# Kernel optimization log

Hardware: AMD Instinct MI355X
Metric: run time of the kernel (lower is better)

Reference implementation:

```python
import jax, jax.numpy as jnp
import numpy as np

B, P, D, H, U, C = 32, 196, 512, 8, 4, 500

def setup_inputs() -> dict:
    key = jax.random.key(0)
    ks = jax.random.split(key, 12)
    s = 0.02
    return {
        "patch_embeddings": jax.random.normal(ks[0], (B, P, D), jnp.float32),
        "global_features": jax.random.normal(ks[1], (B, D), jnp.float32),
        "query_vectors": jax.random.normal(ks[2], (H, D), jnp.float32) * s,
        "dom_W": jax.random.normal(ks[3], (D, D), jnp.float32) / np.sqrt(D),
        "dom_b": jnp.zeros((D,), jnp.float32),
        "sem_W": jax.random.normal(ks[4], (H, D, D), jnp.float32) / np.sqrt(D),
        "sem_b": jnp.zeros((H, D), jnp.float32),
        "unknown_semantic_tokens": jax.random.normal(ks[5], (U, D), jnp.float32) * s,
        "known_prefix": jax.random.normal(ks[6], (C, 1, D), jnp.float32) * s,   # SOS embedding per class
        "known_suffix": jax.random.normal(ks[7], (C, 1, D), jnp.float32) * s,   # last-token embedding per class
        "unk_prefix": jax.random.normal(ks[8], (1, D), jnp.float32) * s,
        "unk_suffix": jax.random.normal(ks[9], (1, D), jnp.float32) * s,
    }


def reference(patch_embeddings, global_features, query_vectors, dom_W, dom_b,
              sem_W, sem_b, unknown_semantic_tokens, known_prefix, known_suffix,
              unk_prefix, unk_suffix):
    b, p, d = patch_embeddings.shape
    h = query_vectors.shape[0]
    c = known_prefix.shape[0]
    u = unknown_semantic_tokens.shape[0]

    # SemanticTokenExtractor: per-head attention over patches (vectorized over heads)
    scores = jnp.einsum('bpd,hd->bph', patch_embeddings, query_vectors)      # [B,P,H]
    weights = jax.nn.softmax(scores, axis=1)                                  # softmax over patches
    semantic_tokens = jnp.einsum('bph,bpd->bhd', weights, patch_embeddings)   # [B,H,D]

    # DomainTokenGenerator (2D input -> identity) + domain projection (torch Linear: x @ W.T + b)
    projected_domain = global_features @ dom_W.T + dom_b                      # [B,D]

    # Per-head semantic projections: head k uses its own Linear
    projected_sem = jnp.einsum('bhd,hed->bhe', semantic_tokens, sem_W) + sem_b  # [B,H,D]

    # Known prompts: for each (b, c): [prefix_c(1), domain_b(1), semantics_b(H), suffix_c(1)]
    pre = jnp.broadcast_to(known_prefix[None], (b, c, 1, d))
    dom = jnp.broadcast_to(projected_domain[:, None, None, :], (b, c, 1, d))
    sem = jnp.broadcast_to(projected_sem[:, None], (b, c, h, d))
    suf = jnp.broadcast_to(known_suffix[None], (b, c, 1, d))
    known_prompts = jnp.concatenate([pre, dom, sem, suf], axis=2).reshape(b * c, h + 3, d)

    # Unknown prompts: [unk_prefix(1), domain_b(1), unknown_semantic_tokens(U), unk_suffix(1)]
    upre = jnp.broadcast_to(unk_prefix[None], (b, 1, d))
    udom = projected_domain[:, None, :]
    usem = jnp.broadcast_to(unknown_semantic_tokens[None], (b, u, d))
    usuf = jnp.broadcast_to(unk_suffix[None], (b, 1, d))
    unknown_prompts = jnp.concatenate([upre, udom, usem, usuf], axis=1)       # [B, U+3, D]

    return known_prompts, unknown_prompts, semantic_tokens
```

## Files before the change

kernel.cpp:

```cpp
#include <hip/hip_runtime.h>

typedef unsigned int uint32;
typedef uint32 v4u __attribute__((ext_vector_type(4)));

#define Bb 32
#define Pp 196
#define Dd 512
#define Hh 8
#define Uu 4
#define Cc 500

#define OUT1_ELEM_OFF 90112000
#define OUT2_ELEM_OFF 90226688

#define WS_SC   0
#define WS_PART 51200
#define WS_DOM  1099776
#define WS_SEM  1116160

__device__ __forceinline__ float dot4(float4 a, float4 b, float acc) {
    acc = fmaf(a.x, b.x, acc);
    acc = fmaf(a.y, b.y, acc);
    acc = fmaf(a.z, b.z, acc);
    acc = fmaf(a.w, b.w, acc);
    return acc;
}

__global__ __launch_bounds__(256)
void k_scores(const float* __restrict__ patch, const float* __restrict__ query,
              float* __restrict__ sc) {
    __shared__ float s_q[Hh * Dd];
    const int b = blockIdx.x / 49;
    const int p0 = (blockIdx.x % 49) * 4;
    const int tid = threadIdx.x;
    for (int j = tid; j < Hh * Dd / 4; j += 256)
        ((float4*)s_q)[j] = ((const float4*)query)[j];
    __syncthreads();

    const int wave = tid >> 6, lane = tid & 63;
    const int p = p0 + wave;
    const float* pr = patch + ((size_t)b * Pp + p) * Dd + lane * 8;
    const float4 v0 = *(const float4*)pr;
    const float4 v1 = *(const float4*)(pr + 4);

    float out = 0.f;
#pragma unroll
    for (int h = 0; h < 8; ++h) {
        const float4 q0 = *(const float4*)&s_q[h * Dd + lane * 8];
        const float4 q1 = *(const float4*)&s_q[h * Dd + lane * 8 + 4];
        float a = dot4(v0, q0, 0.f);
        a = dot4(v1, q1, a);
#pragma unroll
        for (int m = 32; m >= 1; m >>= 1) a += __shfl_xor(a, m, 64);
        if (lane == h) out = a;
    }
    if (lane < 8) sc[((size_t)b * Hh + lane) * Pp + p] = out;
}

__global__ __launch_bounds__(256)
void k_pool_part(const float* __restrict__ patch, const float* __restrict__ sc,
                 float* __restrict__ part) {
    __shared__ float s_w[Hh * Pp];
    const int b = blockIdx.x >> 3;
    const int pc = blockIdx.x & 7;
    const int tid = threadIdx.x;

    for (int j = tid; j < Hh * Pp; j += 256) s_w[j] = sc[(size_t)b * Hh * Pp + j];
    __syncthreads();

    {
        const int h = tid >> 5, gl = tid & 31;
        float m = -1e30f;
        for (int p = gl; p < Pp; p += 32) m = fmaxf(m, s_w[h * Pp + p]);
#pragma unroll
        for (int mm = 16; mm >= 1; mm >>= 1) m = fmaxf(m, __shfl_xor(m, mm, 64));
        float s = 0.f;
        for (int p = gl; p < Pp; p += 32) s += __expf(s_w[h * Pp + p] - m);
#pragma unroll
        for (int mm = 16; mm >= 1; mm >>= 1) s += __shfl_xor(s, mm, 64);
        const float inv = 1.f / s;
        for (int p = gl; p < Pp; p += 32)
            s_w[h * Pp + p] = __expf(s_w[h * Pp + p] - m) * inv;
    }
    __syncthreads();

    const int f = tid & 127;
    const int hq = tid >> 7;
    const int pstart = pc * 25;
    const int pend = (pstart + 25 < Pp) ? pstart + 25 : Pp;
    float4 a0 = {0, 0, 0, 0}, a1 = a0, a2 = a0, a3 = a0;
    const float4* pb4 = (const float4*)(patch + (size_t)b * Pp * Dd);
    for (int p = pstart; p < pend; ++p) {
        const float4 pv = pb4[p * 128 + f];
        const float w0 = s_w[(hq * 4 + 0) * Pp + p];
        const float w1 = s_w[(hq * 4 + 1) * Pp + p];
        const float w2 = s_w[(hq * 4 + 2) * Pp + p];
        const float w3 = s_w[(hq * 4 + 3) * Pp + p];
        a0.x = fmaf(w0, pv.x, a0.x); a0.y = fmaf(w0, pv.y, a0.y);
        a0.z = fmaf(w0, pv.z, a0.z); a0.w = fmaf(w0, pv.w, a0.w);
        a1.x = fmaf(w1, pv.x, a1.x); a1.y = fmaf(w1, pv.y, a1.y);
        a1.z = fmaf(w1, pv.z, a1.z); a1.w = fmaf(w1, pv.w, a1.w);
        a2.x = fmaf(w2, pv.x, a2.x); a2.y = fmaf(w2, pv.y, a2.y);
        a2.z = fmaf(w2, pv.z, a2.z); a2.w = fmaf(w2, pv.w, a2.w);
        a3.x = fmaf(w3, pv.x, a3.x); a3.y = fmaf(w3, pv.y, a3.y);
        a3.z = fmaf(w3, pv.z, a3.z); a3.w = fmaf(w3, pv.w, a3.w);
    }
    float4* po = (float4*)part + ((size_t)b * 8 + pc) * 1024;
    po[(hq * 4 + 0) * 128 + f] = a0;
    po[(hq * 4 + 1) * 128 + f] = a1;
    po[(hq * 4 + 2) * 128 + f] = a2;
    po[(hq * 4 + 3) * 128 + f] = a3;
}

__global__ __launch_bounds__(256)
void k_combine(const float* __restrict__ part, float* __restrict__ st) {
    const int idx = blockIdx.x * 256 + threadIdx.x;
    const int b = idx >> 10;
    const int r = idx & 1023;
    const float4* p4 = (const float4*)part;
    float4 a = {0, 0, 0, 0};
#pragma unroll
    for (int pc = 0; pc < 8; ++pc) {
        const float4 v = p4[((size_t)b * 8 + pc) * 1024 + r];
        a.x += v.x; a.y += v.y; a.z += v.z; a.w += v.w;
    }
    ((float4*)st)[idx] = a;
}

__global__ __launch_bounds__(256)
void k_proj(const float* __restrict__ gf, const float* __restrict__ domW,
            const float* __restrict__ domb, const float* __restrict__ semW,
            const float* __restrict__ semb, const float* __restrict__ st,
            float* __restrict__ dom_ws, float* __restrict__ sem_ws) {
    const int blk = blockIdx.x;
    if (blk < 512) {
        const int tg = blk * 256 + threadIdx.x;
        const int b = tg >> 12;
        const int rem = tg & 4095;
        const int h = rem >> 9;
        const int e = rem & 511;
        const float4* wr = (const float4*)(semW + (size_t)(h * Dd + e) * Dd);
        const float4* sr = (const float4*)(st + (size_t)(b * Hh + h) * Dd);
        float acc = semb[h * Dd + e];
#pragma unroll 8
        for (int j = 0; j < Dd / 4; ++j) acc = dot4(sr[j], wr[j], acc);
        sem_ws[(b * Hh + h) * Dd + e] = acc;
    } else {
        const int tg = (blk - 512) * 256 + threadIdx.x;
        const int b = tg >> 9;
        const int e = tg & 511;
        const float4* wr = (const float4*)(domW + (size_t)e * Dd);
        const float4* gr = (const float4*)(gf + (size_t)b * Dd);
        float acc = domb[e];
#pragma unroll 8
        for (int j = 0; j < Dd / 4; ++j) acc = dot4(gr[j], wr[j], acc);
        dom_ws[b * Dd + e] = acc;
    }
}

__global__ __launch_bounds__(256)
void k_assemble(const v4u* __restrict__ pre, const v4u* __restrict__ suf,
                const v4u* __restrict__ dom, const v4u* __restrict__ sem,
                const v4u* __restrict__ upre, const v4u* __restrict__ usuf,
                const v4u* __restrict__ ust,
                v4u* __restrict__ out0, v4u* __restrict__ out1) {
    const int blk = blockIdx.x;
    const int tid = threadIdx.x;
    if (blk < 1600) {
        const int b = blk / 50;
        const int chunk = blk % 50;
        __shared__ v4u mid[1152];
        for (int j = tid; j < 1152; j += 256)
            mid[j] = (j < 128) ? dom[b * 128 + j] : sem[b * 1024 + (j - 128)];
        __syncthreads();
        const int c0 = chunk * 10;
        for (int r = 0; r < 10; ++r) {
            const int c = c0 + r;
            v4u* row = out0 + (size_t)(b * Cc + c) * 1408;
            for (int i = tid; i < 1408; i += 256) {
                const int t = i >> 7;
                const int off = i & 127;
                v4u v;
                if (t == 0) v = pre[c * 128 + off];
                else if (t == 10) v = suf[c * 128 + off];
                else v = mid[(t - 1) * 128 + off];
                __builtin_nontemporal_store(v, &row[i]);
            }
        }
    } else {
        const int b = blk - 1600;
        for (int i = tid; i < 896; i += 256) {
            const int t = i >> 7;
            const int off = i & 127;
            v4u v;
            if (t == 0) v = upre[off];
            else if (t == 6) v = usuf[off];
            else if (t == 1) v = dom[b * 128 + off];
            else v = ust[(t - 2) * 128 + off];
            __builtin_nontemporal_store(v, &out1[b * 896 + i]);
        }
    }
}

extern "C" void kernel_launch(void* const* d_in, const int* in_sizes, int n_in,
                              void* d_out, int out_size, void* d_ws, size_t ws_size,
                              hipStream_t stream) {
    const float* patch = (const float*)d_in[0];
    const float* gf    = (const float*)d_in[1];
    const float* query = (const float*)d_in[2];
    const float* domW  = (const float*)d_in[3];
    const float* domb  = (const float*)d_in[4];
    const float* semW  = (const float*)d_in[5];
    const float* semb  = (const float*)d_in[6];
    const float* ust   = (const float*)d_in[7];
    const float* pre   = (const float*)d_in[8];
    const float* suf   = (const float*)d_in[9];
    const float* upre  = (const float*)d_in[10];
    const float* usuf  = (const float*)d_in[11];

    float* out = (float*)d_out;
    float* st_out = out + OUT2_ELEM_OFF;

    float* ws   = (float*)d_ws;
    float* sc_w = ws + WS_SC;
    float* part = ws + WS_PART;
    float* domp = ws + WS_DOM;
    float* semp = ws + WS_SEM;

    hipLaunchKernelGGL(k_scores, dim3(Bb * 49), dim3(256), 0, stream, patch, query, sc_w);
    hipLaunchKernelGGL(k_pool_part, dim3(Bb * 8), dim3(256), 0, stream, patch, sc_w, part);
    hipLaunchKernelGGL(k_combine, dim3(128), dim3(256), 0, stream, part, st_out);
    hipLaunchKernelGGL(k_proj, dim3(576), dim3(256), 0, stream,
                       gf, domW, domb, semW, semb, st_out, domp, semp);
    hipLaunchKernelGGL(k_assemble, dim3(1632), dim3(256), 0, stream,
                       (const v4u*)pre, (const v4u*)suf,
                       (const v4u*)domp, (const v4u*)semp,
                       (const v4u*)upre, (const v4u*)usuf, (const v4u*)ust,
                       (v4u*)out, (v4u*)(out + OUT1_ELEM_OFF));
}
```

Baseline: 480.4 us.

## Tile per-head projection through LDS and split pooling into more chunks

The per-head semantic projection now stages a 32-row slice of the head's weight matrix and all 32 batch semantic tokens in padded shared memory. Each thread computes a 2x2 register tile, so each weight is reused across all batches instead of being streamed once per batch from global memory. The pooling stage splits patches into 16 chunks per batch instead of 8, giving more blocks in exchange for more partial-sum traffic in the combine step. The large LDS footprint limits occupancy to one block per CU for the projection.

```diff
diff --git a/kernel.cpp b/kernel.cpp
--- a/kernel.cpp
+++ b/kernel.cpp
@@ -13,10 +13,12 @@
 #define OUT1_ELEM_OFF 90112000
 #define OUT2_ELEM_OFF 90226688
 
+#define NPC 16
+
 #define WS_SC   0
 #define WS_PART 51200
-#define WS_DOM  1099776
-#define WS_SEM  1116160
+#define WS_DOM  2148352
+#define WS_SEM  2164736
 
 __device__ __forceinline__ float dot4(float4 a, float4 b, float acc) {
     acc = fmaf(a.x, b.x, acc);
@@ -61,8 +63,8 @@
 void k_pool_part(const float* __restrict__ patch, const float* __restrict__ sc,
                  float* __restrict__ part) {
     __shared__ float s_w[Hh * Pp];
-    const int b = blockIdx.x >> 3;
-    const int pc = blockIdx.x & 7;
+    const int b = blockIdx.x >> 4;
+    const int pc = blockIdx.x & 15;
     const int tid = threadIdx.x;
 
     for (int j = tid; j < Hh * Pp; j += 256) s_w[j] = sc[(size_t)b * Hh * Pp + j];
@@ -86,8 +88,8 @@
 
     const int f = tid & 127;
     const int hq = tid >> 7;
-    const int pstart = pc * 25;
-    const int pend = (pstart + 25 < Pp) ? pstart + 25 : Pp;
+    const int pstart = pc * 13;
+    const int pend = (pstart + 13 < Pp) ? pstart + 13 : Pp;
     float4 a0 = {0, 0, 0, 0}, a1 = a0, a2 = a0, a3 = a0;
     const float4* pb4 = (const float4*)(patch + (size_t)b * Pp * Dd);
     for (int p = pstart; p < pend; ++p) {
@@ -105,7 +107,7 @@
         a3.x = fmaf(w3, pv.x, a3.x); a3.y = fmaf(w3, pv.y, a3.y);
         a3.z = fmaf(w3, pv.z, a3.z); a3.w = fmaf(w3, pv.w, a3.w);
     }
-    float4* po = (float4*)part + ((size_t)b * 8 + pc) * 1024;
+    float4* po = (float4*)part + ((size_t)b * NPC + pc) * 1024;
     po[(hq * 4 + 0) * 128 + f] = a0;
     po[(hq * 4 + 1) * 128 + f] = a1;
     po[(hq * 4 + 2) * 128 + f] = a2;
@@ -120,33 +122,60 @@
     const float4* p4 = (const float4*)part;
     float4 a = {0, 0, 0, 0};
 #pragma unroll
-    for (int pc = 0; pc < 8; ++pc) {
-        const float4 v = p4[((size_t)b * 8 + pc) * 1024 + r];
+    for (int pc = 0; pc < NPC; ++pc) {
+        const float4 v = p4[((size_t)b * NPC + pc) * 1024 + r];
         a.x += v.x; a.y += v.y; a.z += v.z; a.w += v.w;
     }
     ((float4*)st)[idx] = a;
 }
 
+#define PJS 513
 __global__ __launch_bounds__(256)
 void k_proj(const float* __restrict__ gf, const float* __restrict__ domW,
             const float* __restrict__ domb, const float* __restrict__ semW,
             const float* __restrict__ semb, const float* __restrict__ st,
             float* __restrict__ dom_ws, float* __restrict__ sem_ws) {
+    __shared__ float s_w[32 * PJS];
+    __shared__ float s_st[32 * PJS];
     const int blk = blockIdx.x;
-    if (blk < 512) {
-        const int tg = blk * 256 + threadIdx.x;
-        const int b = tg >> 12;
-        const int rem = tg & 4095;
-        const int h = rem >> 9;
-        const int e = rem & 511;
-        const float4* wr = (const float4*)(semW + (size_t)(h * Dd + e) * Dd);
-        const float4* sr = (const float4*)(st + (size_t)(b * Hh + h) * Dd);
-        float acc = semb[h * Dd + e];
+    const int tid = threadIdx.x;
+    if (blk < 128) {
+        const int h = blk >> 4;
+        const int e0 = (blk & 15) * 32;
+        for (int g = tid; g < 32 * 128; g += 256) {
+            const int r = g >> 7, c4 = g & 127;
+            const float4 w = ((const float4*)semW)[((size_t)(h * Dd + e0 + r)) * 128 + c4];
+            float* dw = &s_w[r * PJS + c4 * 4];
+            dw[0] = w.x; dw[1] = w.y; dw[2] = w.z; dw[3] = w.w;
+            const float4 s = ((const float4*)st)[((size_t)(r * Hh + h)) * 128 + c4];
+            float* ds = &s_st[r * PJS + c4 * 4];
+            ds[0] = s.x; ds[1] = s.y; ds[2] = s.z; ds[3] = s.w;
+        }
+        __syncthreads();
+        const int pe = tid & 15;
+        const int pb = tid >> 4;
+        const float* w0r = &s_w[(2 * pe) * PJS];
+        const float* w1r = &s_w[(2 * pe + 1) * PJS];
+        const float* s0r = &s_st[(2 * pb) * PJS];
+        const float* s1r = &s_st[(2 * pb + 1) * PJS];
+        float a00 = 0.f, a01 = 0.f, a10 = 0.f, a11 = 0.f;
 #pragma unroll 8
-        for (int j = 0; j < Dd / 4; ++j) acc = dot4(sr[j], wr[j], acc);
-        sem_ws[(b * Hh + h) * Dd + e] = acc;
+        for (int d = 0; d < Dd; ++d) {
+            const float w0 = w0r[d], w1 = w1r[d];
+            const float s0 = s0r[d], s1 = s1r[d];
+            a00 = fmaf(s0, w0, a00);
+            a01 = fmaf(s0, w1, a01);
+            a10 = fmaf(s1, w0, a10);
+            a11 = fmaf(s1, w1, a11);
+        }
+        const int e_ = e0 + 2 * pe;
+        const float b0 = semb[h * Dd + e_], b1 = semb[h * Dd + e_ + 1];
+        float* o0 = &sem_ws[((2 * pb) * Hh + h) * Dd + e_];
+        float* o1 = &sem_ws[((2 * pb + 1) * Hh + h) * Dd + e_];
+        o0[0] = a00 + b0; o0[1] = a01 + b1;
+        o1[0] = a10 + b0; o1[1] = a11 + b1;
     } else {
-        const int tg = (blk - 512) * 256 + threadIdx.x;
+        const int tg = (blk - 128) * 256 + tid;
         const int b = tg >> 9;
         const int e = tg & 511;
         const float4* wr = (const float4*)(domW + (size_t)e * Dd);
@@ -228,9 +257,9 @@
     float* semp = ws + WS_SEM;
 
     hipLaunchKernelGGL(k_scores, dim3(Bb * 49), dim3(256), 0, stream, patch, query, sc_w);
-    hipLaunchKernelGGL(k_pool_part, dim3(Bb * 8), dim3(256), 0, stream, patch, sc_w, part);
+    hipLaunchKernelGGL(k_pool_part, dim3(Bb * NPC), dim3(256), 0, stream, patch, sc_w, part);
     hipLaunchKernelGGL(k_combine, dim3(128), dim3(256), 0, stream, part, st_out);
-    hipLaunchKernelGGL(k_proj, dim3(576), dim3(256), 0, stream,
+    hipLaunchKernelGGL(k_proj, dim3(192), dim3(256), 0, stream,
                        gf, domW, domb, semW, semb, st_out, domp, semp);
     hipLaunchKernelGGL(k_assemble, dim3(1632), dim3(256), 0, stream,
                        (const v4u*)pre, (const v4u*)suf,
```

Result: faster. 441.2 us (-8.2%).
